# Kernel tuning notes

Hardware: AMD Instinct MI355X
Metric: run time of the kernel (lower is better)

## Reference

```python
import jax, jax.numpy as jnp
import numpy as np

N_NODES = 100000
N_EDGES = 1600000
N_REL = 8
IN_CH = 128
HID = 64
OUT_CH = 128


def _rgcn_layer(x, src, dst, et, W_rel, W_root, b, num_rel):
    # x: [N, Fin]; W_rel: [R, Fin, Fout]; W_root: [Fin, Fout]; b: [Fout]
    N = x.shape[0]
    # Transform once per relation, then gather per edge (avoids per-edge matmul)
    xt = jnp.einsum('ni,rio->rno', x, W_rel)          # [R, N, Fout]
    msgs = xt[et, src]                                 # [E, Fout]
    # Per-(dst, relation) mean normalization (PyG RGCNConv aggr='mean' per relation)
    seg = dst * num_rel + et                           # combined segment id
    deg = jax.ops.segment_sum(jnp.ones_like(et, dtype=x.dtype), seg,
                              num_segments=N * num_rel)  # [N*R]
    norm = 1.0 / jnp.maximum(deg[seg], 1.0)            # [E]
    agg = jax.ops.segment_sum(msgs * norm[:, None], dst, num_segments=N)  # [N, Fout]
    return agg + x @ W_root + b


def setup_inputs() -> dict:
    key = jax.random.key(0)
    ks = jax.random.split(key, 9)
    x = jax.random.normal(ks[0], (N_NODES, IN_CH), dtype=jnp.float32)
    edge_index = jax.random.randint(ks[1], (2, N_EDGES), 0, N_NODES, dtype=jnp.int64)
    edge_type = jax.random.randint(ks[2], (N_EDGES,), 0, N_REL, dtype=jnp.int64)
    s1 = 1.0 / np.sqrt(IN_CH)
    s2 = 1.0 / np.sqrt(HID)
    W1 = jax.random.uniform(ks[3], (N_REL, IN_CH, HID), jnp.float32, -s1, s1)
    root1 = jax.random.uniform(ks[4], (IN_CH, HID), jnp.float32, -s1, s1)
    b1 = jnp.zeros((HID,), jnp.float32)
    W2 = jax.random.uniform(ks[5], (N_REL, HID, OUT_CH), jnp.float32, -s2, s2)
    root2 = jax.random.uniform(ks[6], (HID, OUT_CH), jnp.float32, -s2, s2)
    b2 = jnp.zeros((OUT_CH,), jnp.float32)
    return {"x": x, "edge_index": edge_index, "edge_type": edge_type,
            "W1": W1, "root1": root1, "b1": b1,
            "W2": W2, "root2": root2, "b2": b2}


def reference(x, edge_index, edge_type, W1, root1, b1, W2, root2, b2):
    src, dst = edge_index[0], edge_index[1]
    h = _rgcn_layer(x, src, dst, edge_type, W1, root1, b1, N_REL)
    h = jax.nn.relu(h)
    out = _rgcn_layer(h, src, dst, edge_type, W2, root2, b2, N_REL)
    return out
```

## Files before the change

### kernel.cpp

```cpp
#include <hip/hip_runtime.h>
#include <cstdint>
#include <cstddef>

#define NREL 8

typedef __attribute__((ext_vector_type(8))) short bfrag8;
typedef __attribute__((ext_vector_type(4))) float facc4;

__device__ __forceinline__ ushort f2bf(float f) {
  union { float f; uint u; } v; v.f = f;
  uint u = v.u + 0x7fffu + ((v.u >> 16) & 1u);
  return (ushort)(u >> 16);
}
__device__ __forceinline__ float bf2f(ushort u) {
  union { uint u; float f; } v; v.u = ((uint)u) << 16;
  return v.f;
}
__device__ __forceinline__ float readlane_f(float v, int l) {
  union { float f; int i; } u; u.f = v;
  u.i = __builtin_amdgcn_readlane(u.i, l);
  return u.f;
}

__global__ __launch_bounds__(256) void cvt_all_kernel(const float* __restrict__ W1,
                                                      const float* __restrict__ r1,
                                                      const float* __restrict__ W2,
                                                      const float* __restrict__ r2,
                                                      ushort* __restrict__ W1t,
                                                      ushort* __restrict__ r1t,
                                                      ushort* __restrict__ W2t,
                                                      ushort* __restrict__ r2t) {
  int idx = blockIdx.x * 256 + threadIdx.x;
  const float* in; ushort* out; int K, N, rel;
  if (idx < 65536)        { in = W1; out = W1t; K = 128; N = 64;  rel = idx >> 13; idx &= 8191; }
  else if (idx < 73728)   { idx -= 65536; in = r1; out = r1t; K = 128; N = 64; rel = 0; }
  else if (idx < 139264)  { idx -= 73728; in = W2; out = W2t; K = 64; N = 128; rel = idx >> 13; idx &= 8191; }
  else if (idx < 147456)  { idx -= 139264; in = r2; out = r2t; K = 64; N = 128; rel = 0; }
  else return;
  int n = idx / K, k = idx - n * K;
  out[(size_t)rel * K * N + (size_t)n * K + k] =
      f2bf(in[(size_t)rel * K * N + (size_t)k * N + n]);
}

__global__ __launch_bounds__(256) void fused1_kernel(const float* __restrict__ x,
                                                     const ushort* __restrict__ W1t,
                                                     const ushort* __restrict__ r1t,
                                                     ushort* __restrict__ xt,
                                                     float* __restrict__ hroot,
                                                     const int* __restrict__ dst,
                                                     const int* __restrict__ et,
                                                     uint* __restrict__ hist,
                                                     uint* __restrict__ rank,
                                                     int M, int E, int HB) {
  __shared__ __align__(16) ushort Bws[64][136];
  const int bid = blockIdx.x;
  const int hq = bid / 3;
  if ((bid % 3) == 0 && hq < HB) {
    int base = (hq * 256 + threadIdx.x) * 8;
    if (base + 8 <= E) {
      int4 d0 = *(const int4*)&dst[base], d1 = *(const int4*)&dst[base + 4];
      int4 r0 = *(const int4*)&et[base],  r1 = *(const int4*)&et[base + 4];
      int dd[8] = {d0.x, d0.y, d0.z, d0.w, d1.x, d1.y, d1.z, d1.w};
      int rr[8] = {r0.x, r0.y, r0.z, r0.w, r1.x, r1.y, r1.z, r1.w};
      uint rk[8];
#pragma unroll
      for (int j = 0; j < 8; ++j)
        rk[j] = atomicAdd(&hist[(size_t)rr[j] * M + dd[j]], 1u);
      *(uint4*)&rank[base] = make_uint4(rk[0], rk[1], rk[2], rk[3]);
      *(uint4*)&rank[base + 4] = make_uint4(rk[4], rk[5], rk[6], rk[7]);
    } else {
      for (int j = 0; base + j < E; ++j)
        rank[base + j] = atomicAdd(&hist[(size_t)et[base + j] * M + dst[base + j]], 1u);
    }
    return;
  }
  const int gidx = (hq < HB) ? (bid - hq - 1) : (bid - HB);
  const int tid = threadIdx.x;
  const int w = tid >> 6, l = tid & 63;
  const int rows0 = gidx * 64;
  const int mrow = w * 16 + (l & 15);
  const int koff = (l >> 4) * 8;
  const int m = rows0 + mrow;
  const int mc = (m < M) ? m : (M - 1);
  bfrag8 xf[4];
#pragma unroll
  for (int kc = 0; kc < 4; ++kc) {
    float4 a = *(const float4*)&x[(size_t)mc * 128 + kc * 32 + koff];
    float4 b = *(const float4*)&x[(size_t)mc * 128 + kc * 32 + koff + 4];
    union { bfrag8 f; ushort4 u[2]; } pk;
    pk.u[0] = make_ushort4(f2bf(a.x), f2bf(a.y), f2bf(a.z), f2bf(a.w));
    pk.u[1] = make_ushort4(f2bf(b.x), f2bf(b.y), f2bf(b.z), f2bf(b.w));
    xf[kc] = pk.f;
  }
  for (int r = 0; r < 9; ++r) {
    __syncthreads();
    const ushort* Wsrc = (r < 8) ? (W1t + (size_t)r * 64 * 128) : r1t;
#pragma unroll
    for (int i = 0; i < 8; ++i) {
      int g = tid + 256 * i;
      int row = g >> 5, c4 = (g & 31) * 4;
      *(ushort4*)&Bws[row][c4] = *(const ushort4*)&Wsrc[(size_t)row * 128 + c4];
    }
    __syncthreads();
#pragma unroll
    for (int ct = 0; ct < 4; ++ct) {
      facc4 acc = {0.f, 0.f, 0.f, 0.f};
#pragma unroll
      for (int kc = 0; kc < 4; ++kc) {
        bfrag8 af = *(const bfrag8*)&Bws[ct * 16 + (l & 15)][kc * 32 + koff];
        acc = __builtin_amdgcn_mfma_f32_16x16x32_bf16(af, xf[kc], acc, 0, 0, 0);
      }
      if (m < M) {
        int n0 = ct * 16 + (l >> 4) * 4;
        if (r < 8) {
          *(ushort4*)&xt[(size_t)m * 512 + r * 64 + n0] =
              make_ushort4(f2bf(acc[0]), f2bf(acc[1]), f2bf(acc[2]), f2bf(acc[3]));
        } else {
          *(float4*)&hroot[(size_t)m * 64 + n0] =
              make_float4(acc[0], acc[1], acc[2], acc[3]);
        }
      }
    }
  }
}

__global__ __launch_bounds__(256) void scan1_kernel(const uint* __restrict__ hist,
                                                    uint* __restrict__ bsum, int M) {
  __shared__ uint r[256];
  int b = blockIdx.x, t = threadIdx.x;
  int d = b * 256 + t;
  uint s = 0;
  if (d < M) {
#pragma unroll
    for (int i = 0; i < 8; ++i) s += hist[(size_t)i * M + d];
  }
  r[t] = s; __syncthreads();
  for (int dd = 128; dd > 0; dd >>= 1) { if (t < dd) r[t] += r[t + dd]; __syncthreads(); }
  if (t == 0) bsum[b] = r[0];
}

__global__ __launch_bounds__(512) void scan2_kernel(uint* __restrict__ bsum, int nb) {
  __shared__ uint s[512];
  int t = threadIdx.x;
  uint v = (t < nb) ? bsum[t] : 0u;
  s[t] = v;
  __syncthreads();
  for (int d = 1; d < 512; d <<= 1) {
    uint add = (t >= d) ? s[t - d] : 0u;
    __syncthreads();
    s[t] += add;
    __syncthreads();
  }
  if (t < nb) bsum[t] = s[t] - v;
}

__global__ __launch_bounds__(256) void scan3_kernel(const uint* __restrict__ hist,
                                                    const uint* __restrict__ bsum,
                                                    uint* __restrict__ off,
                                                    float* __restrict__ idg,
                                                    int M, int E) {
  __shared__ uint ts[256];
  int b = blockIdx.x, t = threadIdx.x;
  int d = b * 256 + t;
  uint h[8]; uint sum = 0;
#pragma unroll
  for (int i = 0; i < 8; ++i) { h[i] = (d < M) ? hist[(size_t)i * M + d] : 0u; sum += h[i]; }
  ts[t] = sum;
  __syncthreads();
  uint own = sum;
  for (int dd = 1; dd < 256; dd <<= 1) {
    uint add = (t >= dd) ? ts[t - dd] : 0u;
    __syncthreads();
    ts[t] += add;
    __syncthreads();
  }
  uint run = bsum[b] + (ts[t] - own);
  if (d < M) {
#pragma unroll
    for (int i = 0; i < 8; ++i) {
      int k = d * 8 + i;
      off[k] = run;
      idg[k] = 1.0f / fmaxf((float)h[i], 1.0f);
      run += h[i];
    }
    if (d == M - 1) off[M * 8] = (uint)E;
  }
}

__global__ __launch_bounds__(256) void place_kernel(const int* __restrict__ src,
                                                    const int* __restrict__ dst,
                                                    const int* __restrict__ et,
                                                    const uint* __restrict__ off,
                                                    const uint* __restrict__ rank,
                                                    uint* __restrict__ sp, int E) {
  int base = (blockIdx.x * 256 + threadIdx.x) * 8;
  if (base + 8 <= E) {
    int4 d0 = *(const int4*)&dst[base], d1 = *(const int4*)&dst[base + 4];
    int4 r0 = *(const int4*)&et[base],  r1 = *(const int4*)&et[base + 4];
    int4 s0 = *(const int4*)&src[base], s1 = *(const int4*)&src[base + 4];
    uint4 k0 = *(const uint4*)&rank[base], k1 = *(const uint4*)&rank[base + 4];
    int dd[8] = {d0.x, d0.y, d0.z, d0.w, d1.x, d1.y, d1.z, d1.w};
    int rr[8] = {r0.x, r0.y, r0.z, r0.w, r1.x, r1.y, r1.z, r1.w};
    int ss[8] = {s0.x, s0.y, s0.z, s0.w, s1.x, s1.y, s1.z, s1.w};
    uint kk[8] = {k0.x, k0.y, k0.z, k0.w, k1.x, k1.y, k1.z, k1.w};
    uint oo[8];
#pragma unroll
    for (int j = 0; j < 8; ++j) oo[j] = off[(size_t)dd[j] * NREL + rr[j]];
#pragma unroll
    for (int j = 0; j < 8; ++j)
      sp[oo[j] + kk[j]] = ((uint)ss[j] << 7) | ((uint)rr[j] << 4);
  } else {
    for (int j = 0; base + j < E; ++j) {
      int e = base + j;
      int r = et[e];
      sp[off[(size_t)dst[e] * NREL + r] + rank[e]] = ((uint)src[e] << 7) | ((uint)r << 4);
    }
  }
}

__global__ __launch_bounds__(256) void agg1_kernel(const uint* __restrict__ off,
                                                   const uint* __restrict__ sp,
                                                   const float* __restrict__ idg,
                                                   const ushort* __restrict__ xt,
                                                   const float* __restrict__ hroot,
                                                   const float* __restrict__ b1,
                                                   ushort* __restrict__ hb, int N) {
  int wid = (blockIdx.x * 256 + threadIdx.x) >> 6;
  if (wid >= N) return;
  int lane = threadIdx.x & 63;
  uint lane2 = (uint)lane * 2u;
  uint e0 = (uint)__builtin_amdgcn_readfirstlane((int)off[(size_t)wid * 8]);
  uint e1 = (uint)__builtin_amdgcn_readfirstlane((int)off[(size_t)wid * 8 + 8]);
  float idgl = (lane < 8) ? idg[(size_t)wid * 8 + lane] : 0.f;
  const char* xb = (const char*)xt;
  float acct = 0.f, accs = 0.f;
  uint cur = 0;
  for (uint b0 = e0; b0 < e1; b0 += 64) {
    uint vsp = sp[b0 + lane];
    uint vpr = __shfl(vsp, ((int)lane - 1) & 63);
    unsigned long long bmv = __ballot(((vsp ^ vpr) & 0x70u) != 0u);
    uint blo = (uint)__builtin_amdgcn_readfirstlane((int)(uint)bmv);
    uint bhi = (uint)__builtin_amdgcn_readfirstlane((int)(uint)(bmv >> 32));
    uint f0  = (uint)__builtin_amdgcn_readlane((int)vsp, 0);
    if ((b0 == e0) || (((f0 ^ cur) & 0x70u) != 0u)) blo |= 1u; else blo &= ~1u;
    unsigned long long sbm = (((unsigned long long)bhi) << 32) | blo;
    int n = min(64, (int)(e1 - b0));
    int i = 0;
    for (; i + 8 <= n; i += 8) {
      uint p[8]; float v[8];
#pragma unroll
      for (int j = 0; j < 8; ++j)
        p[j] = (uint)__builtin_amdgcn_readlane((int)vsp, i + j);
#pragma unroll
      for (int j = 0; j < 8; ++j)
        v[j] = bf2f(*(const ushort*)(xb + (size_t)((p[j] << 3) + lane2)));
#pragma unroll
      for (int j = 0; j < 8; ++j) {
        if ((sbm >> j) & 1ull) {
          acct += accs * readlane_f(idgl, (int)((cur >> 4) & 7u));
          accs = 0.f; cur = p[j];
        }
        accs += v[j];
      }
      sbm >>= 8;
    }
    for (; i < n; ++i) {
      uint pp = (uint)__builtin_amdgcn_readlane((int)vsp, i);
      float vv = bf2f(*(const ushort*)(xb + (size_t)((pp << 3) + lane2)));
      if (sbm & 1ull) {
        acct += accs * readlane_f(idgl, (int)((cur >> 4) & 7u));
        accs = 0.f; cur = pp;
      }
      sbm >>= 1;
      accs += vv;
    }
  }
  acct += accs * readlane_f(idgl, (int)((cur >> 4) & 7u));
  float h = fmaxf(acct + hroot[(size_t)wid * 64 + lane] + b1[lane], 0.f);
  hb[(size_t)wid * 64 + lane] = f2bf(h);
}

__global__ __launch_bounds__(256) void agg2_kernel(const uint* __restrict__ off,
                                                   const uint* __restrict__ sp,
                                                   const float* __restrict__ idg,
                                                   const ushort* __restrict__ hb,
                                                   ushort* __restrict__ y2, int N) {
  int wid = (blockIdx.x * 256 + threadIdx.x) >> 6;
  if (wid >= N) return;
  int lane = threadIdx.x & 63;
  uint lane2 = (uint)lane * 2u;
  uint e0 = (uint)__builtin_amdgcn_readfirstlane((int)off[(size_t)wid * 8]);
  uint e1 = (uint)__builtin_amdgcn_readfirstlane((int)off[(size_t)wid * 8 + 8]);
  float idgl = (lane < 8) ? idg[(size_t)wid * 8 + lane] : 0.f;
  const char* hbb = (const char*)hb;
  float accs = 0.f;
  uint cur = 0;
  bool live = false;
  uint written = 0;
  for (uint b0 = e0; b0 < e1; b0 += 64) {
    uint vsp = sp[b0 + lane];
    uint vpr = __shfl(vsp, ((int)lane - 1) & 63);
    unsigned long long bmv = __ballot(((vsp ^ vpr) & 0x70u) != 0u);
    uint blo = (uint)__builtin_amdgcn_readfirstlane((int)(uint)bmv);
    uint bhi = (uint)__builtin_amdgcn_readfirstlane((int)(uint)(bmv >> 32));
    uint f0  = (uint)__builtin_amdgcn_readlane((int)vsp, 0);
    if ((b0 == e0) || (((f0 ^ cur) & 0x70u) != 0u)) blo |= 1u; else blo &= ~1u;
    unsigned long long sbm = (((unsigned long long)bhi) << 32) | blo;
    int n = min(64, (int)(e1 - b0));
    int i = 0;
    for (; i + 8 <= n; i += 8) {
      uint p[8]; float v[8];
#pragma unroll
      for (int j = 0; j < 8; ++j)
        p[j] = (uint)__builtin_amdgcn_readlane((int)vsp, i + j);
#pragma unroll
      for (int j = 0; j < 8; ++j)
        v[j] = bf2f(*(const ushort*)(hbb + (size_t)((p[j] & ~127u) + lane2)));
#pragma unroll
      for (int j = 0; j < 8; ++j) {
        if ((sbm >> j) & 1ull) {
          if (live) {
            int r = (int)((cur >> 4) & 7u);
            y2[(size_t)wid * 512 + r * 64 + lane] = f2bf(accs * readlane_f(idgl, r));
            written |= 1u << r;
          }
          accs = 0.f; cur = p[j]; live = true;
        }
        accs += v[j];
      }
      sbm >>= 8;
    }
    for (; i < n; ++i) {
      uint pp = (uint)__builtin_amdgcn_readlane((int)vsp, i);
      float vv = bf2f(*(const ushort*)(hbb + (size_t)((pp & ~127u) + lane2)));
      if (sbm & 1ull) {
        if (live) {
          int r = (int)((cur >> 4) & 7u);
          y2[(size_t)wid * 512 + r * 64 + lane] = f2bf(accs * readlane_f(idgl, r));
          written |= 1u << r;
        }
        accs = 0.f; cur = pp; live = true;
      }
      sbm >>= 1;
      accs += vv;
    }
  }
  if (live) {
    int r = (int)((cur >> 4) & 7u);
    y2[(size_t)wid * 512 + r * 64 + lane] = f2bf(accs * readlane_f(idgl, r));
    written |= 1u << r;
  }
#pragma unroll
  for (int r = 0; r < 8; ++r)
    if (!((written >> r) & 1u))
      y2[(size_t)wid * 512 + r * 64 + lane] = 0;
}

__global__ __launch_bounds__(256) void gemm_out_kernel(const ushort* __restrict__ hb,
                                                       const ushort* __restrict__ y2,
                                                       const ushort* __restrict__ W2t,
                                                       const ushort* __restrict__ r2t,
                                                       const float* __restrict__ b2,
                                                       float* __restrict__ out, int M) {
  __shared__ __align__(16) ushort Bws[128][72];
  const int tid = threadIdx.x;
  const int w = tid >> 6, l = tid & 63;
  const int rows0 = blockIdx.x * 64;
  const int mrow = w * 16 + (l & 15);
  const int koff = (l >> 4) * 8;
  const int m = rows0 + mrow;
  const int mc = (m < M) ? m : (M - 1);
  facc4 oacc[8] = {};
#pragma unroll
  for (int i = 0; i < 8; ++i) {
    int g = tid + 256 * i;
    int row = g >> 4, c4 = (g & 15) * 4;
    *(ushort4*)&Bws[row][c4] = *(const ushort4*)&r2t[(size_t)row * 64 + c4];
  }
  __syncthreads();
  {
    bfrag8 h0 = *(const bfrag8*)&hb[(size_t)mc * 64 + koff];
    bfrag8 h1 = *(const bfrag8*)&hb[(size_t)mc * 64 + 32 + koff];
#pragma unroll
    for (int ct = 0; ct < 8; ++ct) {
      bfrag8 a0 = *(const bfrag8*)&Bws[ct * 16 + (l & 15)][koff];
      bfrag8 a1 = *(const bfrag8*)&Bws[ct * 16 + (l & 15)][32 + koff];
      oacc[ct] = __builtin_amdgcn_mfma_f32_16x16x32_bf16(a0, h0, oacc[ct], 0, 0, 0);
      oacc[ct] = __builtin_amdgcn_mfma_f32_16x16x32_bf16(a1, h1, oacc[ct], 0, 0, 0);
    }
  }
  for (int r = 0; r < NREL; ++r) {
    __syncthreads();
#pragma unroll
    for (int i = 0; i < 8; ++i) {
      int g = tid + 256 * i;
      int row = g >> 4, c4 = (g & 15) * 4;
      *(ushort4*)&Bws[row][c4] = *(const ushort4*)&W2t[((size_t)r * 128 + row) * 64 + c4];
    }
    __syncthreads();
    bfrag8 y0 = *(const bfrag8*)&y2[(size_t)mc * 512 + r * 64 + koff];
    bfrag8 y1f = *(const bfrag8*)&y2[(size_t)mc * 512 + r * 64 + 32 + koff];
#pragma unroll
    for (int ct = 0; ct < 8; ++ct) {
      bfrag8 a0 = *(const bfrag8*)&Bws[ct * 16 + (l & 15)][koff];
      bfrag8 a1 = *(const bfrag8*)&Bws[ct * 16 + (l & 15)][32 + koff];
      oacc[ct] = __builtin_amdgcn_mfma_f32_16x16x32_bf16(a0, y0, oacc[ct], 0, 0, 0);
      oacc[ct] = __builtin_amdgcn_mfma_f32_16x16x32_bf16(a1, y1f, oacc[ct], 0, 0, 0);
    }
  }
  if (m < M) {
#pragma unroll
    for (int ct = 0; ct < 8; ++ct) {
      int n0 = ct * 16 + (l >> 4) * 4;
      float4 bb = *(const float4*)&b2[n0];
      float4 o = make_float4(oacc[ct][0] + bb.x, oacc[ct][1] + bb.y,
                             oacc[ct][2] + bb.z, oacc[ct][3] + bb.w);
      *(float4*)&out[(size_t)m * 128 + n0] = o;
    }
  }
}

extern "C" void kernel_launch(void* const* d_in, const int* in_sizes, int n_in,
                              void* d_out, int out_size, void* d_ws, size_t ws_size,
                              hipStream_t stream) {
  const float* x     = (const float*)d_in[0];
  const int*   ei    = (const int*)d_in[1];
  const int*   et    = (const int*)d_in[2];
  const float* W1    = (const float*)d_in[3];
  const float* root1 = (const float*)d_in[4];
  const float* b1    = (const float*)d_in[5];
  const float* W2    = (const float*)d_in[6];
  const float* root2 = (const float*)d_in[7];
  const float* b2    = (const float*)d_in[8];
  float* out = (float*)d_out;

  const int M = in_sizes[0] / 128;
  const int E = in_sizes[2];
  const int NS = M * NREL;
  const int* srcp = ei;
  const int* dstp = ei + E;

  auto align = [](char*& p, size_t n) { char* q = p; p += (n + 255) & ~(size_t)255; return q; };
  char* p = (char*)d_ws;
  ushort* xt    = (ushort*)align(p, (size_t)M * 512 * 2);
  float*  hroot = (float*) align(p, (size_t)M * 64 * 4);
  ushort* hb    = (ushort*)align(p, (size_t)M * 64 * 2);
  uint*   hist  = (uint*)  align(p, (size_t)NS * 4);
  uint*   rank  = (uint*)  align(p, (size_t)E * 4);
  uint*   off   = (uint*)  align(p, (size_t)(NS + 1) * 4);
  float*  idg   = (float*) align(p, (size_t)NS * 4);
  uint*   sp    = (uint*)  align(p, (size_t)(E + 64) * 4);
  uint*   bsum  = (uint*)  align(p, 4096);
  ushort* W1t   = (ushort*)align(p, (size_t)NREL * 64 * 128 * 2);
  ushort* r1t   = (ushort*)align(p, (size_t)64 * 128 * 2);
  ushort* W2t   = (ushort*)align(p, (size_t)NREL * 128 * 64 * 2);
  ushort* r2t   = (ushort*)align(p, (size_t)128 * 64 * 2);
  ushort* y2 = xt;

  cvt_all_kernel<<<(147456 + 255) / 256, 256, 0, stream>>>(W1, root1, W2, root2,
                                                           W1t, r1t, W2t, r2t);
  hipMemsetAsync(hist, 0, (size_t)NS * 4, stream);

  const int E8B  = (int)(((long long)E + 8LL * 256 - 1) / (8LL * 256));
  const int MB64 = (M + 63) / 64;
  fused1_kernel<<<E8B + MB64, 256, 0, stream>>>(x, W1t, r1t, xt, hroot, dstp, et,
                                                hist, rank, M, E, E8B);

  const int NB = (M + 255) / 256;
  scan1_kernel<<<NB, 256, 0, stream>>>(hist, bsum, M);
  scan2_kernel<<<1, 512, 0, stream>>>(bsum, NB);
  scan3_kernel<<<NB, 256, 0, stream>>>(hist, bsum, off, idg, M, E);
  place_kernel<<<E8B, 256, 0, stream>>>(srcp, dstp, et, off, rank, sp, E);

  const int AGB = (M * 64 + 255) / 256;

  agg1_kernel<<<AGB, 256, 0, stream>>>(off, sp, idg, xt, hroot, b1, hb, M);

  agg2_kernel<<<AGB, 256, 0, stream>>>(off, sp, idg, hb, y2, M);
  gemm_out_kernel<<<MB64, 256, 0, stream>>>(hb, y2, W2t, r2t, b2, out, M);
}
```

Before: 327.5 us.

## Regroup kernels: fuse histogram with weight convert, placement with layer-1 GEMM

Result: slower. 345.8 us (+5.6%).

```diff
diff --git a/kernel.cpp b/kernel.cpp
--- a/kernel.cpp
+++ b/kernel.cpp
@@ -22,15 +22,40 @@
   return u.f;
 }
 
-__global__ __launch_bounds__(256) void cvt_all_kernel(const float* __restrict__ W1,
-                                                      const float* __restrict__ r1,
-                                                      const float* __restrict__ W2,
-                                                      const float* __restrict__ r2,
-                                                      ushort* __restrict__ W1t,
-                                                      ushort* __restrict__ r1t,
-                                                      ushort* __restrict__ W2t,
-                                                      ushort* __restrict__ r2t) {
-  int idx = blockIdx.x * 256 + threadIdx.x;
+__global__ __launch_bounds__(256) void k1_hist_cvt(const int* __restrict__ dst,
+                                                   const int* __restrict__ et,
+                                                   uint* __restrict__ hist,
+                                                   uint* __restrict__ rank,
+                                                   const float* __restrict__ W1,
+                                                   const float* __restrict__ r1,
+                                                   const float* __restrict__ W2,
+                                                   const float* __restrict__ r2,
+                                                   ushort* __restrict__ W1t,
+                                                   ushort* __restrict__ r1t,
+                                                   ushort* __restrict__ W2t,
+                                                   ushort* __restrict__ r2t,
+                                                   int M, int E, int HB) {
+  const int bid = blockIdx.x;
+  if (bid < HB) {
+    int base = (bid * 256 + threadIdx.x) * 8;
+    if (base + 8 <= E) {
+      int4 d0 = *(const int4*)&dst[base], d1 = *(const int4*)&dst[base + 4];
+      int4 r0 = *(const int4*)&et[base],  r1v = *(const int4*)&et[base + 4];
+      int dd[8] = {d0.x, d0.y, d0.z, d0.w, d1.x, d1.y, d1.z, d1.w};
+      int rr[8] = {r0.x, r0.y, r0.z, r0.w, r1v.x, r1v.y, r1v.z, r1v.w};
+      uint rk[8];
+#pragma unroll
+      for (int j = 0; j < 8; ++j)
+        rk[j] = atomicAdd(&hist[(size_t)rr[j] * M + dd[j]], 1u);
+      *(uint4*)&rank[base] = make_uint4(rk[0], rk[1], rk[2], rk[3]);
+      *(uint4*)&rank[base + 4] = make_uint4(rk[4], rk[5], rk[6], rk[7]);
+    } else {
+      for (int j = 0; base + j < E; ++j)
+        rank[base + j] = atomicAdd(&hist[(size_t)et[base + j] * M + dst[base + j]], 1u);
+    }
+    return;
+  }
+  int idx = (bid - HB) * 256 + threadIdx.x;
   const float* in; ushort* out; int K, N, rel;
   if (idx < 65536)        { in = W1; out = W1t; K = 128; N = 64;  rel = idx >> 13; idx &= 8191; }
   else if (idx < 73728)   { idx -= 65536; in = r1; out = r1t; K = 128; N = 64; rel = 0; }
@@ -42,39 +67,111 @@
       f2bf(in[(size_t)rel * K * N + (size_t)k * N + n]);
 }
 
-__global__ __launch_bounds__(256) void fused1_kernel(const float* __restrict__ x,
+__global__ __launch_bounds__(256) void scan1_kernel(const uint* __restrict__ hist,
+                                                    uint* __restrict__ bsum, int M) {
+  __shared__ uint r[256];
+  int b = blockIdx.x, t = threadIdx.x;
+  int d = b * 256 + t;
+  uint s = 0;
+  if (d < M) {
+#pragma unroll
+    for (int i = 0; i < 8; ++i) s += hist[(size_t)i * M + d];
+  }
+  r[t] = s; __syncthreads();
+  for (int dd = 128; dd > 0; dd >>= 1) { if (t < dd) r[t] += r[t + dd]; __syncthreads(); }
+  if (t == 0) bsum[b] = r[0];
+}
+
+__global__ __launch_bounds__(512) void scan2_kernel(uint* __restrict__ bsum, int nb) {
+  __shared__ uint s[512];
+  int t = threadIdx.x;
+  uint v = (t < nb) ? bsum[t] : 0u;
+  s[t] = v;
+  __syncthreads();
+  for (int d = 1; d < 512; d <<= 1) {
+    uint add = (t >= d) ? s[t - d] : 0u;
+    __syncthreads();
+    s[t] += add;
+    __syncthreads();
+  }
+  if (t < nb) bsum[t] = s[t] - v;
+}
+
+__global__ __launch_bounds__(256) void scan3_kernel(const uint* __restrict__ hist,
+                                                    const uint* __restrict__ bsum,
+                                                    uint* __restrict__ off,
+                                                    float* __restrict__ idg,
+                                                    int M, int E) {
+  __shared__ uint ts[256];
+  int b = blockIdx.x, t = threadIdx.x;
+  int d = b * 256 + t;
+  uint h[8]; uint sum = 0;
+#pragma unroll
+  for (int i = 0; i < 8; ++i) { h[i] = (d < M) ? hist[(size_t)i * M + d] : 0u; sum += h[i]; }
+  ts[t] = sum;
+  __syncthreads();
+  uint own = sum;
+  for (int dd = 1; dd < 256; dd <<= 1) {
+    uint add = (t >= dd) ? ts[t - dd] : 0u;
+    __syncthreads();
+    ts[t] += add;
+    __syncthreads();
+  }
+  uint run = bsum[b] + (ts[t] - own);
+  if (d < M) {
+#pragma unroll
+    for (int i = 0; i < 8; ++i) {
+      int k = d * 8 + i;
+      off[k] = run;
+      idg[k] = 1.0f / fmaxf((float)h[i], 1.0f);
+      run += h[i];
+    }
+    if (d == M - 1) off[M * 8] = (uint)E;
+  }
+}
+
+__global__ __launch_bounds__(256) void k5_place_gemm(const int* __restrict__ src,
+                                                     const int* __restrict__ dst,
+                                                     const int* __restrict__ et,
+                                                     const uint* __restrict__ off,
+                                                     const uint* __restrict__ rank,
+                                                     uint* __restrict__ sp,
+                                                     const float* __restrict__ x,
                                                      const ushort* __restrict__ W1t,
                                                      const ushort* __restrict__ r1t,
                                                      ushort* __restrict__ xt,
                                                      float* __restrict__ hroot,
-                                                     const int* __restrict__ dst,
-                                                     const int* __restrict__ et,
-                                                     uint* __restrict__ hist,
-                                                     uint* __restrict__ rank,
-                                                     int M, int E, int HB) {
+                                                     int M, int E, int PB) {
   __shared__ __align__(16) ushort Bws[64][136];
   const int bid = blockIdx.x;
   const int hq = bid / 3;
-  if ((bid % 3) == 0 && hq < HB) {
+  if ((bid % 3) == 0 && hq < PB) {
     int base = (hq * 256 + threadIdx.x) * 8;
     if (base + 8 <= E) {
       int4 d0 = *(const int4*)&dst[base], d1 = *(const int4*)&dst[base + 4];
-      int4 r0 = *(const int4*)&et[base],  r1 = *(const int4*)&et[base + 4];
+      int4 r0 = *(const int4*)&et[base],  r1v = *(const int4*)&et[base + 4];
+      int4 s0 = *(const int4*)&src[base], s1 = *(const int4*)&src[base + 4];
+      uint4 k0 = *(const uint4*)&rank[base], k1 = *(const uint4*)&rank[base + 4];
       int dd[8] = {d0.x, d0.y, d0.z, d0.w, d1.x, d1.y, d1.z, d1.w};
-      int rr[8] = {r0.x, r0.y, r0.z, r0.w, r1.x, r1.y, r1.z, r1.w};
-      uint rk[8];
-#pragma unroll
-      for (int j = 0; j < 8; ++j)
-        rk[j] = atomicAdd(&hist[(size_t)rr[j] * M + dd[j]], 1u);
-      *(uint4*)&rank[base] = make_uint4(rk[0], rk[1], rk[2], rk[3]);
-      *(uint4*)&rank[base + 4] = make_uint4(rk[4], rk[5], rk[6], rk[7]);
+      int rr[8] = {r0.x, r0.y, r0.z, r0.w, r1v.x, r1v.y, r1v.z, r1v.w};
+      int ss[8] = {s0.x, s0.y, s0.z, s0.w, s1.x, s1.y, s1.z, s1.w};
+      uint kk[8] = {k0.x, k0.y, k0.z, k0.w, k1.x, k1.y, k1.z, k1.w};
+      uint oo[8];
+#pragma unroll
+      for (int j = 0; j < 8; ++j) oo[j] = off[(size_t)dd[j] * NREL + rr[j]];
+#pragma unroll
+      for (int j = 0; j < 8; ++j)
+        sp[oo[j] + kk[j]] = ((uint)ss[j] << 7) | ((uint)rr[j] << 4);
     } else {
-      for (int j = 0; base + j < E; ++j)
-        rank[base + j] = atomicAdd(&hist[(size_t)et[base + j] * M + dst[base + j]], 1u);
+      for (int j = 0; base + j < E; ++j) {
+        int e = base + j;
+        int r = et[e];
+        sp[off[(size_t)dst[e] * NREL + r] + rank[e]] = ((uint)src[e] << 7) | ((uint)r << 4);
+      }
     }
     return;
   }
-  const int gidx = (hq < HB) ? (bid - hq - 1) : (bid - HB);
+  const int gidx = (hq < PB) ? (bid - hq - 1) : (bid - PB);
   const int tid = threadIdx.x;
   const int w = tid >> 6, l = tid & 63;
   const int rows0 = gidx * 64;
@@ -120,100 +217,6 @@
               make_float4(acc[0], acc[1], acc[2], acc[3]);
         }
       }
-    }
-  }
-}
-
-__global__ __launch_bounds__(256) void scan1_kernel(const uint* __restrict__ hist,
-                                                    uint* __restrict__ bsum, int M) {
-  __shared__ uint r[256];
-  int b = blockIdx.x, t = threadIdx.x;
-  int d = b * 256 + t;
-  uint s = 0;
-  if (d < M) {
-#pragma unroll
-    for (int i = 0; i < 8; ++i) s += hist[(size_t)i * M + d];
-  }
-  r[t] = s; __syncthreads();
-  for (int dd = 128; dd > 0; dd >>= 1) { if (t < dd) r[t] += r[t + dd]; __syncthreads(); }
-  if (t == 0) bsum[b] = r[0];
-}
-
-__global__ __launch_bounds__(512) void scan2_kernel(uint* __restrict__ bsum, int nb) {
-  __shared__ uint s[512];
-  int t = threadIdx.x;
-  uint v = (t < nb) ? bsum[t] : 0u;
-  s[t] = v;
-  __syncthreads();
-  for (int d = 1; d < 512; d <<= 1) {
-    uint add = (t >= d) ? s[t - d] : 0u;
-    __syncthreads();
-    s[t] += add;
-    __syncthreads();
-  }
-  if (t < nb) bsum[t] = s[t] - v;
-}
-
-__global__ __launch_bounds__(256) void scan3_kernel(const uint* __restrict__ hist,
-                                                    const uint* __restrict__ bsum,
-                                                    uint* __restrict__ off,
-                                                    float* __restrict__ idg,
-                                                    int M, int E) {
-  __shared__ uint ts[256];
-  int b = blockIdx.x, t = threadIdx.x;
-  int d = b * 256 + t;
-  uint h[8]; uint sum = 0;
-#pragma unroll
-  for (int i = 0; i < 8; ++i) { h[i] = (d < M) ? hist[(size_t)i * M + d] : 0u; sum += h[i]; }
-  ts[t] = sum;
-  __syncthreads();
-  uint own = sum;
-  for (int dd = 1; dd < 256; dd <<= 1) {
-    uint add = (t >= dd) ? ts[t - dd] : 0u;
-    __syncthreads();
-    ts[t] += add;
-    __syncthreads();
-  }
-  uint run = bsum[b] + (ts[t] - own);
-  if (d < M) {
-#pragma unroll
-    for (int i = 0; i < 8; ++i) {
-      int k = d * 8 + i;
-      off[k] = run;
-      idg[k] = 1.0f / fmaxf((float)h[i], 1.0f);
-      run += h[i];
-    }
-    if (d == M - 1) off[M * 8] = (uint)E;
-  }
-}
-
-__global__ __launch_bounds__(256) void place_kernel(const int* __restrict__ src,
-                                                    const int* __restrict__ dst,
-                                                    const int* __restrict__ et,
-                                                    const uint* __restrict__ off,
-                                                    const uint* __restrict__ rank,
-                                                    uint* __restrict__ sp, int E) {
-  int base = (blockIdx.x * 256 + threadIdx.x) * 8;
-  if (base + 8 <= E) {
-    int4 d0 = *(const int4*)&dst[base], d1 = *(const int4*)&dst[base + 4];
-    int4 r0 = *(const int4*)&et[base],  r1 = *(const int4*)&et[base + 4];
-    int4 s0 = *(const int4*)&src[base], s1 = *(const int4*)&src[base + 4];
-    uint4 k0 = *(const uint4*)&rank[base], k1 = *(const uint4*)&rank[base + 4];
-    int dd[8] = {d0.x, d0.y, d0.z, d0.w, d1.x, d1.y, d1.z, d1.w};
-    int rr[8] = {r0.x, r0.y, r0.z, r0.w, r1.x, r1.y, r1.z, r1.w};
-    int ss[8] = {s0.x, s0.y, s0.z, s0.w, s1.x, s1.y, s1.z, s1.w};
-    uint kk[8] = {k0.x, k0.y, k0.z, k0.w, k1.x, k1.y, k1.z, k1.w};
-    uint oo[8];
-#pragma unroll
-    for (int j = 0; j < 8; ++j) oo[j] = off[(size_t)dd[j] * NREL + rr[j]];
-#pragma unroll
-    for (int j = 0; j < 8; ++j)
-      sp[oo[j] + kk[j]] = ((uint)ss[j] << 7) | ((uint)rr[j] << 4);
-  } else {
-    for (int j = 0; base + j < E; ++j) {
-      int e = base + j;
-      int r = et[e];
-      sp[off[(size_t)dst[e] * NREL + r] + rank[e]] = ((uint)src[e] << 7) | ((uint)r << 4);
     }
   }
 }
@@ -457,20 +460,22 @@
   ushort* r2t   = (ushort*)align(p, (size_t)128 * 64 * 2);
   ushort* y2 = xt;
 
-  cvt_all_kernel<<<(147456 + 255) / 256, 256, 0, stream>>>(W1, root1, W2, root2,
-                                                           W1t, r1t, W2t, r2t);
   hipMemsetAsync(hist, 0, (size_t)NS * 4, stream);
 
   const int E8B  = (int)(((long long)E + 8LL * 256 - 1) / (8LL * 256));
-  const int MB64 = (M + 63) / 64;
-  fused1_kernel<<<E8B + MB64, 256, 0, stream>>>(x, W1t, r1t, xt, hroot, dstp, et,
-                                                hist, rank, M, E, E8B);
+  const int CVB  = (147456 + 255) / 256;
+  k1_hist_cvt<<<E8B + CVB, 256, 0, stream>>>(dstp, et, hist, rank,
+                                             W1, root1, W2, root2,
+                                             W1t, r1t, W2t, r2t, M, E, E8B);
 
   const int NB = (M + 255) / 256;
   scan1_kernel<<<NB, 256, 0, stream>>>(hist, bsum, M);
   scan2_kernel<<<1, 512, 0, stream>>>(bsum, NB);
   scan3_kernel<<<NB, 256, 0, stream>>>(hist, bsum, off, idg, M, E);
-  place_kernel<<<E8B, 256, 0, stream>>>(srcp, dstp, et, off, rank, sp, E);
+
+  const int MB64 = (M + 63) / 64;
+  k5_place_gemm<<<E8B + MB64, 256, 0, stream>>>(srcp, dstp, et, off, rank, sp,
+                                                x, W1t, r1t, xt, hroot, M, E, E8B);
 
   const int AGB = (M * 64 + 255) / 256;
 
```
